# Kernel optimization log

Hardware: AMD Instinct MI355X
Metric: run time of the kernel (lower is better)

The kernel has to match this reference:

```python
import jax, jax.numpy as jnp
import numpy as np

B, C, N = 8, 128, 4096  # (batch, channels=dim, time); F = N//2+1 = 2049 (odd)


def setup_inputs() -> dict:
    key = jax.random.key(0)
    ks = jax.random.split(key, 7)
    s = 1.0 / np.sqrt(C)
    return {
        "x_in": jax.random.normal(ks[0], (B, C, N), dtype=jnp.float32),
        "W_K": jax.random.normal(ks[1], (C, C), dtype=jnp.float32) * s,
        "b_K": jax.random.normal(ks[2], (C,), dtype=jnp.float32) * s,
        "W_V": jax.random.normal(ks[3], (C, C), dtype=jnp.float32) * s,
        "b_V": jax.random.normal(ks[4], (C,), dtype=jnp.float32) * s,
        "w_high": jax.random.normal(ks[5], (C, 2), dtype=jnp.float32) * 0.02,
        "threshold_param": jax.random.uniform(ks[6], (1,), dtype=jnp.float32) * 0.5,
    }


def reference(x_in, W_K, b_K, W_V, b_V, w_high, threshold_param):
    x = jnp.transpose(x_in, (0, 2, 1)).astype(jnp.float32)  # (B, N, C)
    _, n, c = x.shape
    x_fft = jnp.fft.rfft(x, axis=1, norm="ortho")            # (B, F, C) complex64
    K = jnp.fft.rfft(x @ W_K.T + b_K, axis=1, norm="ortho")  # (B, F, C)
    V = jnp.fft.rfft(x @ W_V.T + b_V, axis=1, norm="ortho")  # (B, F, C)
    scale = c ** (-0.5)
    # complex attention scores (no conjugation, matching torch.matmul(Q, K^T))
    attn = jnp.einsum("bfc,bgc->bfg", x_fft, K) * scale      # (B, F, F) complex
    attn = jax.nn.softmax(jnp.abs(attn), axis=-1)            # real softmax of |scores|
    context = jnp.einsum("bfg,bgc->bfc", attn.astype(x_fft.dtype), V)
    # adaptive high-frequency mask
    energy = jnp.sum(jnp.abs(x_fft) ** 2, axis=-1)           # (B, F)
    median_energy = jnp.median(energy, axis=1, keepdims=True)
    normalized = energy / (median_energy + 1e-6)
    threshold = jnp.quantile(normalized, threshold_param[0])  # global quantile
    mask = (normalized > threshold)[:, :, None]               # (B, F, 1)
    w_hi = w_high[:, 0] + 1j * w_high[:, 1]                   # (C,) complex
    context = context + jnp.where(mask, x_fft, 0.0) * w_hi
    out = jnp.fft.irfft(context, n=n, axis=1, norm="ortho")  # (B, N, C) float32
    return jnp.transpose(out, (0, 2, 1))                      # (B, C, N)
```

## Files before the change

### kernel.cpp

```cpp
#include <hip/hip_runtime.h>
#include <math.h>

#define NB 8
#define NC 128
#define NT 4096
#define NF 2049
#define FP 2176

typedef __bf16 bf16;
typedef __bf16 bf16x2 __attribute__((ext_vector_type(2)));
typedef __bf16 bf16x8 __attribute__((ext_vector_type(8)));
typedef float f32x4 __attribute__((ext_vector_type(4)));
typedef unsigned int uint32x4 __attribute__((ext_vector_type(4)));

__device__ __forceinline__ void async16(const bf16* g, bf16* l) {
    __builtin_amdgcn_global_load_lds(
        (const __attribute__((address_space(1))) void*)g,
        (__attribute__((address_space(3))) void*)l, 16, 0, 0);
}

__device__ __forceinline__ bf16x8 derive_b2(bf16x8 v) {
    uint32x4 u = __builtin_bit_cast(uint32x4, v);
#pragma unroll
    for (int i = 0; i < 4; ++i)
        u[i] = (((u[i] >> 16) | (u[i] << 16)) ^ 0x00008000u);
    return __builtin_bit_cast(bf16x8, u);
}

__device__ __forceinline__ float2 cmulf(float2 a, float2 b) {
    return make_float2(a.x * b.x - a.y * b.y, a.x * b.y + a.y * b.x);
}

__global__ __launch_bounds__(256) void twiddle_kernel(float2* __restrict__ tw) {
    int k = blockIdx.x * 256 + threadIdx.x;
    if (k < 2048) {
        float ang = (float)M_PI * (float)k * (1.0f / 2048.0f);
        float sw, cw;
        __sincosf(ang, &sw, &cw);
        tw[k] = make_float2(cw, -sw);
    }
}

__device__ __forceinline__ void fft4096(float2* buf, const float2* __restrict__ tw) {
    int sh = 0;
#pragma unroll
    for (int s6 = 0; s6 < 6; ++s6) {
        int L = 1 << sh;
        __syncthreads();
        for (int t = threadIdx.x; t < 1024; t += 256) {
            int pos = t & (L - 1);
            int base = ((t >> sh) << (sh + 2)) + pos;
            int k1 = pos << (10 - sh);
            float2 w1 = tw[k1];
            float2 w2 = tw[2 * k1];
            float2 w3 = cmulf(w1, w2);
            float2 x0 = buf[base];
            float2 x1 = cmulf(buf[base + L], w1);
            float2 x2 = cmulf(buf[base + 2 * L], w2);
            float2 x3 = cmulf(buf[base + 3 * L], w3);
            float2 b0 = make_float2(x0.x + x2.x, x0.y + x2.y);
            float2 b1 = make_float2(x0.x - x2.x, x0.y - x2.y);
            float2 b2 = make_float2(x1.x + x3.x, x1.y + x3.y);
            float2 b3 = make_float2(x1.x - x3.x, x1.y - x3.y);
            buf[base]         = make_float2(b0.x + b2.x, b0.y + b2.y);
            buf[base + L]     = make_float2(b1.x + b3.y, b1.y - b3.x);
            buf[base + 2 * L] = make_float2(b0.x - b2.x, b0.y - b2.y);
            buf[base + 3 * L] = make_float2(b1.x - b3.y, b1.y + b3.x);
        }
        sh += 2;
    }
    __syncthreads();
}

__device__ __forceinline__ unsigned dr4(unsigned i) {
    unsigned r = __brev(i) >> 20;
    return ((r & 0x555u) << 1) | ((r & 0xAAAu) >> 1);
}

__global__ __launch_bounds__(256) void fft_fwd_kernel(const float* __restrict__ x_in,
                                                      const float2* __restrict__ tw,
                                                      float2* __restrict__ Xc) {
    __shared__ float2 buf[NT];
    int bc = blockIdx.x;
    const float* xrow = x_in + (size_t)bc * NT;
    for (int i = threadIdx.x; i < NT; i += 256)
        buf[dr4((unsigned)i)] = make_float2(xrow[i], 0.0f);
    fft4096(buf, tw);
    const float inv = 1.0f / 64.0f;
    float2* orow = Xc + (size_t)bc * NF;
    for (int f = threadIdx.x; f < NF; f += 256) {
        float2 v = buf[f];
        orow[f] = make_float2(v.x * inv, v.y * inv);
    }
}

__global__ __launch_bounds__(256) void xt_kernel(const float2* __restrict__ Xc,
                                                 float2* __restrict__ Xf2,
                                                 bf16* __restrict__ Xb,
                                                 float* __restrict__ Ep) {
    __shared__ float2 tile[64][65];
    int blk = blockIdx.x;
    int b = blk / 68;
    int t2 = blk % 68;
    int chalf = t2 / 34;
    int c0 = chalf * 64;
    int f0 = (t2 % 34) * 64;
    int t = threadIdx.x;
    int fl = t & 63, cc = t >> 6;
#pragma unroll
    for (int cb = 0; cb < 16; ++cb) {
        int cl = cb * 4 + cc;
        int f = f0 + fl;
        float2 v = make_float2(0.f, 0.f);
        if (f < NF) v = Xc[((size_t)b * NC + c0 + cl) * NF + f];
        tile[fl][cl] = v;
    }
    __syncthreads();
    int chl = t & 63, ww = t >> 6;
    float epart[16];
#pragma unroll
    for (int wb = 0; wb < 16; ++wb) {
        int fl2 = wb * 4 + ww;
        int f = f0 + fl2;
        float2 v = tile[fl2][chl];
        epart[wb] = v.x * v.x + v.y * v.y;
        if (f < NF) Xf2[((size_t)b * NF + f) * 128 + c0 + chl] = v;
        bf16x2 p;
        p[0] = (bf16)v.x; p[1] = (bf16)v.y;
        *(bf16x2*)&Xb[((size_t)b * FP + f) * 256 + 2 * (c0 + chl)] = p;
    }
    __syncthreads();
    float* es = (float*)tile;
#pragma unroll
    for (int wb = 0; wb < 16; ++wb)
        es[(wb * 4 + ww) * 65 + chl] = epart[wb];
    __syncthreads();
    if (t < 64 && f0 + t < NF) {
        float s = 0.f;
#pragma unroll
        for (int c = 0; c < 64; ++c) s += es[t * 65 + c];
        Ep[((size_t)b * 2 + chalf) * FP + f0 + t] = s;
    }
}

__global__ __launch_bounds__(256) void wpack_kernel(const float* __restrict__ W_K,
                                                    const float* __restrict__ W_V,
                                                    bf16* __restrict__ Wk1,
                                                    bf16* __restrict__ Av) {
    int idx = blockIdx.x * 256 + threadIdx.x;
    if (idx < 256 * 256) {
        int n = idx >> 8, k = idx & 255;
        int c = k >> 1;
        int j = n >> 1;
        float v = 0.f;
        if (!(n & 1) && !(k & 1)) v = W_K[j * NC + c];
        else if ((n & 1) && (k & 1)) v = -W_K[j * NC + c];
        Wk1[idx] = (bf16)v;
        float v2 = 0.f;
        if (!(n & 1) && !(k & 1)) v2 = W_V[j * NC + c];
        else if ((n & 1) && (k & 1)) v2 = W_V[j * NC + c];
        Av[idx] = (bf16)v2;
    }
}

__global__ __launch_bounds__(256, 2) void kvgemm_kernel(const bf16* __restrict__ Xb,
                                                        const bf16* __restrict__ Wk1,
                                                        bf16* __restrict__ K1) {
    __shared__ __align__(16) bf16 As[128 * 64];
    __shared__ __align__(16) bf16 Bs[128 * 64];
    int blk = blockIdx.x;
    int b = blk & 7;
    int t2 = blk >> 3;
    int g0 = (t2 >> 1) * 128;
    int n0 = (t2 & 1) * 128;
    int tid = threadIdx.x;
    int wave = tid >> 6, lane = tid & 63;
    int m = lane & 15, quad = lane >> 4;
    int row_off = (wave & 1) * 64, col_off = (wave >> 1) * 64;
    int lrow = lane >> 3;
    int cswz = (lane & 7) ^ lrow;
    int mk = m & 7;

    f32x4 acc[4][4] = {};
    const bf16* Abase = Xb + ((size_t)b * FP + g0) * 256;
    const bf16* Bbase = Wk1 + (size_t)n0 * 256;

    for (int kk = 0; kk < 256; kk += 64) {
        __syncthreads();
#pragma unroll
        for (int t = 0; t < 4; ++t) {
            int r0 = wave * 32 + t * 8;
            async16(Abase + (size_t)(r0 + lrow) * 256 + kk + cswz * 8, As + r0 * 64);
            async16(Bbase + (size_t)(r0 + lrow) * 256 + kk + cswz * 8, Bs + r0 * 64);
        }
        __syncthreads();
#pragma unroll
        for (int k2 = 0; k2 < 64; k2 += 32) {
            bf16x8 a[4], bb[4];
            int pos = (((k2 >> 3) + quad) ^ mk) << 3;
#pragma unroll
            for (int i = 0; i < 4; ++i) a[i] = *(const bf16x8*)&As[(row_off + i * 16 + m) * 64 + pos];
#pragma unroll
            for (int j = 0; j < 4; ++j) bb[j] = *(const bf16x8*)&Bs[(col_off + j * 16 + m) * 64 + pos];
#pragma unroll
            for (int i = 0; i < 4; ++i)
#pragma unroll
                for (int j = 0; j < 4; ++j)
                    acc[i][j] = __builtin_amdgcn_mfma_f32_16x16x32_bf16(a[i], bb[j], acc[i][j], 0, 0, 0);
        }
    }
#pragma unroll
    for (int i = 0; i < 4; ++i)
#pragma unroll
        for (int j = 0; j < 4; ++j)
#pragma unroll
            for (int r = 0; r < 4; ++r) {
                int row = g0 + row_off + i * 16 + quad * 4 + r;
                int col = n0 + col_off + j * 16 + m;
                K1[((size_t)b * FP + row) * 256 + col] = (bf16)acc[i][j][r];
            }
}

__global__ __launch_bounds__(256, 2) void vtgemm_kernel(const bf16* __restrict__ Av,
                                                        const bf16* __restrict__ Xb,
                                                        bf16* __restrict__ Vt) {
    __shared__ __align__(16) bf16 As[128 * 64];
    __shared__ __align__(16) bf16 Bs[128 * 64];
    int blk = blockIdx.x;
    int b = blk & 7;
    int t2 = blk >> 3;
    int g0 = (t2 >> 1) * 128;
    int n0 = (t2 & 1) * 128;
    int tid = threadIdx.x;
    int wave = tid >> 6, lane = tid & 63;
    int m = lane & 15, quad = lane >> 4;
    int row_off = (wave & 1) * 64, col_off = (wave >> 1) * 64;
    int lrow = lane >> 3;
    int cswz = (lane & 7) ^ lrow;
    int mk = m & 7;

    f32x4 acc[4][4] = {};
    const bf16* Abase = Av + (size_t)n0 * 256;
    const bf16* Bbase = Xb + ((size_t)b * FP + g0) * 256;

    for (int kk = 0; kk < 256; kk += 64) {
        __syncthreads();
#pragma unroll
        for (int t = 0; t < 4; ++t) {
            int r0 = wave * 32 + t * 8;
            async16(Abase + (size_t)(r0 + lrow) * 256 + kk + cswz * 8, As + r0 * 64);
            async16(Bbase + (size_t)(r0 + lrow) * 256 + kk + cswz * 8, Bs + r0 * 64);
        }
        __syncthreads();
#pragma unroll
        for (int k2 = 0; k2 < 64; k2 += 32) {
            bf16x8 a[4], bb[4];
            int pos = (((k2 >> 3) + quad) ^ mk) << 3;
#pragma unroll
            for (int i = 0; i < 4; ++i) a[i] = *(const bf16x8*)&As[(row_off + i * 16 + m) * 64 + pos];
#pragma unroll
            for (int j = 0; j < 4; ++j) bb[j] = *(const bf16x8*)&Bs[(col_off + j * 16 + m) * 64 + pos];
#pragma unroll
            for (int i = 0; i < 4; ++i)
#pragma unroll
                for (int j = 0; j < 4; ++j)
                    acc[i][j] = __builtin_amdgcn_mfma_f32_16x16x32_bf16(a[i], bb[j], acc[i][j], 0, 0, 0);
        }
    }
#pragma unroll
    for (int i = 0; i < 4; ++i)
#pragma unroll
        for (int j = 0; j < 4; ++j)
#pragma unroll
            for (int r = 0; r < 4; ++r) {
                int row = n0 + row_off + i * 16 + quad * 4 + r;
                int col = g0 + col_off + j * 16 + m;
                Vt[((size_t)b * 256 + row) * FP + col] = (bf16)acc[i][j][r];
            }
}

__global__ __launch_bounds__(128) void biasfix_kernel(const float* __restrict__ b_K,
                                                      const float* __restrict__ b_V,
                                                      bf16* __restrict__ K1,
                                                      bf16* __restrict__ Vt) {
    int b = blockIdx.x;
    int j = threadIdx.x;
    float bk = 64.0f * b_K[j], bv = 64.0f * b_V[j];
    size_t o = (size_t)b * FP * 256;
    K1[o + 2 * j] = (bf16)((float)K1[o + 2 * j] + bk);
    size_t ov = ((size_t)b * 256 + 2 * j) * FP;
    Vt[ov] = (bf16)((float)Vt[ov] + bv);
}

__global__ __launch_bounds__(256) void median_kernel(const float* __restrict__ Ep,
                                                     float* __restrict__ med) {
    int blk = blockIdx.x;
    int b = blk / 9, chunk = blk % 9;
    __shared__ __align__(16) float e[2052];
    const float* e0 = Ep + (size_t)b * 2 * FP;
    const float* e1 = e0 + FP;
    for (int i = threadIdx.x; i < 2052; i += 256)
        e[i] = (i < NF) ? (e0[i] + e1[i]) : INFINITY;
    __syncthreads();
    int i = chunk * 256 + threadIdx.x;
    float ei = (i < NF) ? e[i] : 0.f;
    int rank = 0;
#pragma unroll 4
    for (int j4 = 0; j4 < 513; ++j4) {
        float4 v = ((const float4*)e)[j4];
        int j = j4 * 4;
        rank += (v.x < ei) || (v.x == ei && j + 0 < i);
        rank += (v.y < ei) || (v.y == ei && j + 1 < i);
        rank += (v.z < ei) || (v.z == ei && j + 2 < i);
        rank += (v.w < ei) || (v.w == ei && j + 3 < i);
    }
    if (i < NF && rank == 1024) med[b] = ei;
}

__global__ __launch_bounds__(256) void norm_kernel(const float* __restrict__ Ep,
                                                   const float* __restrict__ med,
                                                   float* __restrict__ nrm) {
    int idx = blockIdx.x * 256 + threadIdx.x;
    if (idx >= NB * NF) return;
    int b = idx / NF, f = idx % NF;
    float e = Ep[((size_t)b * 2) * FP + f] + Ep[((size_t)b * 2 + 1) * FP + f];
    nrm[idx] = e / (med[b] + 1e-6f);
}

__global__ __launch_bounds__(256) void rankpart_kernel(const float* __restrict__ nrm,
                                                       int* __restrict__ rankpart) {
    const int n = NB * NF;
    int cb = blockIdx.x / 17;
    int chunk = blockIdx.x % 17;
    __shared__ __align__(16) float cdata[1024];
    int base = chunk * 1024;
    for (int t = threadIdx.x; t < 1024; t += 256)
        cdata[t] = (base + t < n) ? nrm[base + t] : INFINITY;
    __syncthreads();
    int i = cb * 256 + threadIdx.x;
    if (i >= n) return;
    float ei = nrm[i];
    int rank = 0;
#pragma unroll 8
    for (int t4 = 0; t4 < 256; ++t4) {
        float4 v = ((const float4*)cdata)[t4];
        int j = base + t4 * 4;
        rank += (v.x < ei) || (v.x == ei && j + 0 < i);
        rank += (v.y < ei) || (v.y == ei && j + 1 < i);
        rank += (v.z < ei) || (v.z == ei && j + 2 < i);
        rank += (v.w < ei) || (v.w == ei && j + 3 < i);
    }
    rankpart[(size_t)i * 17 + chunk] = rank;
}

__global__ __launch_bounds__(256) void rankreduce_kernel(const int* __restrict__ rankpart,
                                                         const float* __restrict__ nrm,
                                                         const float* __restrict__ q,
                                                         float* __restrict__ vk) {
    const int n = NB * NF;
    int i = blockIdx.x * 256 + threadIdx.x;
    if (i >= n) return;
    int rank = 0;
    const int* rp = rankpart + (size_t)i * 17;
#pragma unroll
    for (int c = 0; c < 17; ++c) rank += rp[c];
    double pos = (double)q[0] * (double)(n - 1);
    int k0 = (int)floor(pos);
    int k1 = min(k0 + 1, n - 1);
    if (rank == k0) vk[0] = nrm[i];
    if (rank == k1) vk[1] = nrm[i];
}

__global__ void thresh_kernel(const float* __restrict__ vk,
                              const float* __restrict__ q,
                              float* __restrict__ thr) {
    if (threadIdx.x == 0 && blockIdx.x == 0) {
        const int n = NB * NF;
        double pos = (double)q[0] * (double)(n - 1);
        double k0 = floor(pos);
        double frac = pos - k0;
        thr[0] = (float)((double)vk[0] + ((double)vk[1] - (double)vk[0]) * frac);
    }
}

__global__ __launch_bounds__(256, 3) void score_kernel(const bf16* __restrict__ Xb,
                                                       const bf16* __restrict__ K1,
                                                       bf16* __restrict__ S,
                                                       float* __restrict__ Mpart,
                                                       float* __restrict__ Lpart) {
    __shared__ __align__(16) char smem[24576];
    bf16* As  = (bf16*)smem;
    bf16* B1s = (bf16*)(smem + 16384);
    int blk = blockIdx.x;
    int b = blk & 7;
    int t2 = blk >> 3;
    int f0 = (t2 / 34) * 128;
    int gblk = t2 % 34;
    int g0 = gblk * 64;
    int tid = threadIdx.x;
    int wave = tid >> 6, lane = tid & 63;
    int m = lane & 15, quad = lane >> 4;
    int row_off = (wave & 1) * 64, col_off = (wave >> 1) * 32;

    f32x4 accRe[4][2] = {};
    f32x4 accIm[4][2] = {};
    const bf16* Abase = Xb + ((size_t)b * FP + f0) * 256;
    const bf16* Kbase = K1 + ((size_t)b * FP + g0) * 256;
    int lrow = lane >> 3;
    int cswz = (lane & 7) ^ lrow;
    int mk = m & 7;

    for (int kk = 0; kk < 256; kk += 64) {
        __syncthreads();
#pragma unroll
        for (int t = 0; t < 4; ++t) {
            int r0 = wave * 32 + t * 8;
            async16(Abase + (size_t)(r0 + lrow) * 256 + kk + cswz * 8, As + r0 * 64);
        }
#pragma unroll
        for (int t = 0; t < 2; ++t) {
            int r0 = wave * 16 + t * 8;
            async16(Kbase + (size_t)(r0 + lrow) * 256 + kk + cswz * 8, B1s + r0 * 64);
        }
        __syncthreads();
#pragma unroll
        for (int k2 = 0; k2 < 64; k2 += 32) {
            bf16x8 a[4], b1[2], b2[2];
            int pos = (((k2 >> 3) + quad) ^ mk) << 3;
#pragma unroll
            for (int i = 0; i < 4; ++i)
                a[i] = *(const bf16x8*)&As[(row_off + i * 16 + m) * 64 + pos];
#pragma unroll
            for (int j = 0; j < 2; ++j) {
                b1[j] = *(const bf16x8*)&B1s[(col_off + j * 16 + m) * 64 + pos];
                b2[j] = derive_b2(b1[j]);
            }
#pragma unroll
            for (int i = 0; i < 4; ++i)
#pragma unroll
                for (int j = 0; j < 2; ++j) {
                    accRe[i][j] = __builtin_amdgcn_mfma_f32_16x16x32_bf16(a[i], b1[j], accRe[i][j], 0, 0, 0);
                    accIm[i][j] = __builtin_amdgcn_mfma_f32_16x16x32_bf16(a[i], b2[j], accIm[i][j], 0, 0, 0);
                }
        }
    }
    const float SCALE = 0.08838834764831845f;
    __syncthreads();
    bf16 (*Cs)[76] = (bf16(*)[76])smem;
#pragma unroll
    for (int i = 0; i < 4; ++i)
#pragma unroll
        for (int j = 0; j < 2; ++j)
#pragma unroll
            for (int r = 0; r < 4; ++r) {
                float re = accRe[i][j][r], im = accIm[i][j][r];
                Cs[row_off + i * 16 + quad * 4 + r][col_off + j * 16 + m] =
                    (bf16)(sqrtf(re * re + im * im) * SCALE);
            }
    __syncthreads();
    float* mred = (float*)(smem + 19456);
    float* lred = (float*)(smem + 20480);
    bf16* Sb = S + (size_t)b * FP * FP;
    int row = tid >> 1, half = tid & 1;
    const bf16* src = &Cs[row][half * 32];
    bf16* dst = Sb + (size_t)(f0 + row) * FP + g0 + half * 32;
    int gbase = g0 + half * 32;
    float vf[32];
#pragma unroll
    for (int u = 0; u < 4; ++u) {
        bf16x8 v8 = *(const bf16x8*)&src[u * 8];
        *(bf16x8*)&dst[u * 8] = v8;
#pragma unroll
        for (int e = 0; e < 8; ++e) vf[u * 8 + e] = (float)v8[e];
    }
    if (gblk >= 32) {
#pragma unroll
        for (int k = 0; k < 32; ++k)
            if (gbase + k > 2048) vf[k] = -1e30f;
    }
    float lmax = -1e30f;
#pragma unroll
    for (int k = 0; k < 32; ++k) lmax = fmaxf(lmax, vf[k]);
    mred[tid] = lmax;
    __syncthreads();
    float rmax = fmaxf(mred[row * 2], mred[row * 2 + 1]);
    float lsum = 0.f;
#pragma unroll
    for (int k = 0; k < 32; ++k) lsum += __expf(vf[k] - rmax);
    lred[tid] = lsum;
    __syncthreads();
    if (half == 0) {
        size_t ro = ((size_t)b * FP + f0 + row) * 34 + gblk;
        Mpart[ro] = rmax;
        Lpart[ro] = lred[row * 2] + lred[row * 2 + 1];
    }
}

__global__ __launch_bounds__(256) void rowstat_kernel(const float* __restrict__ Mpart,
                                                      const float* __restrict__ Lpart,
                                                      float* __restrict__ Crow) {
    int row = blockIdx.x * 256 + threadIdx.x;
    if (row >= NB * FP) return;
    const float* mp = Mpart + (size_t)row * 34;
    const float* lp = Lpart + (size_t)row * 34;
    float M = -1e30f;
#pragma unroll
    for (int i = 0; i < 34; ++i) M = fmaxf(M, mp[i]);
    float L = 0.f;
#pragma unroll
    for (int i = 0; i < 34; ++i) L += lp[i] * __expf(mp[i] - M);
    Crow[row] = M + __logf(L);
}

__global__ __launch_bounds__(256) void context_kernel(const bf16* __restrict__ Sg,
                                                      const float* __restrict__ Crow,
                                                      const bf16* __restrict__ Vt,
                                                      float* __restrict__ Ctx) {
    __shared__ __align__(16) bf16 Ps[32 * 64];
    __shared__ __align__(16) bf16 Vs[256 * 64];
    int blk = blockIdx.x;
    int b = blk & 7;
    int f0 = (blk >> 3) * 32;
    int tid = threadIdx.x;
    int wave = tid >> 6, lane = tid & 63;
    int m = lane & 15, quad = lane >> 4;
    int col_off = wave * 64;
    int lrow = lane >> 3;
    int cswz = (lane & 7) ^ lrow;
    int mk = m & 7;

    f32x4 acc[2][4] = {};
    int prow = wave * 8 + lrow;
    const bf16* Prow = Sg + ((size_t)b * FP + f0 + prow) * FP;
    float cst = Crow[(size_t)b * FP + f0 + prow];
    const bf16* Vbase = Vt + (size_t)b * 256 * FP;

    for (int kk = 0; kk < FP; kk += 64) {
        __syncthreads();
#pragma unroll
        for (int t = 0; t < 8; ++t) {
            int r0 = wave * 64 + t * 8;
            async16(Vbase + (size_t)(r0 + lrow) * FP + kk + cswz * 8, Vs + r0 * 64);
        }
        {
            bf16x8 s8 = *(const bf16x8*)&Prow[kk + cswz * 8];
            bf16x8 p8;
#pragma unroll
            for (int e = 0; e < 8; ++e) p8[e] = (bf16)__expf((float)s8[e] - cst);
            *(bf16x8*)&Ps[prow * 64 + (lane & 7) * 8] = p8;
        }
        __syncthreads();
#pragma unroll
        for (int k2 = 0; k2 < 64; k2 += 32) {
            bf16x8 a[2], bb[4];
            int pos = (((k2 >> 3) + quad) ^ mk) << 3;
#pragma unroll
            for (int i = 0; i < 2; ++i) a[i] = *(const bf16x8*)&Ps[(i * 16 + m) * 64 + pos];
#pragma unroll
            for (int j = 0; j < 4; ++j) bb[j] = *(const bf16x8*)&Vs[(col_off + j * 16 + m) * 64 + pos];
#pragma unroll
            for (int i = 0; i < 2; ++i)
#pragma unroll
                for (int j = 0; j < 4; ++j)
                    acc[i][j] = __builtin_amdgcn_mfma_f32_16x16x32_bf16(a[i], bb[j], acc[i][j], 0, 0, 0);
        }
    }
#pragma unroll
    for (int i = 0; i < 2; ++i)
#pragma unroll
        for (int j = 0; j < 4; ++j)
#pragma unroll
            for (int r = 0; r < 4; ++r) {
                int row = f0 + i * 16 + quad * 4 + r;
                int col = col_off + j * 16 + m;
                if (row < NF) Ctx[((size_t)b * NF + row) * 256 + col] = acc[i][j][r];
            }
}

__global__ __launch_bounds__(256) void ctxt_kernel(const float2* __restrict__ Ctx2,
                                                   const float2* __restrict__ Xf2,
                                                   const float* __restrict__ nrm,
                                                   const float* __restrict__ thr,
                                                   const float* __restrict__ w_high,
                                                   float* __restrict__ Ctxt) {
    __shared__ float2 tile[64][33];
    int blk = blockIdx.x;
    int b = blk / 132;
    int t2 = blk % 132;
    int cp0 = (t2 / 33) * 32;
    int f0 = (t2 % 33) * 64;
    int t = threadIdx.x;
    float thrv = thr[0];
    int cpl = t & 31, rr = t >> 5;
#pragma unroll
    for (int rb = 0; rb < 8; ++rb) {
        int fl = rb * 8 + rr;
        int f = f0 + fl;
        float2 v = make_float2(0.f, 0.f);
        if (f < NF) {
            size_t idx = ((size_t)b * NF + f) * 128 + cp0 + cpl;
            v = Ctx2[idx];
            if (nrm[b * NF + f] > thrv) {
                float2 x = Xf2[idx];
                int c = cp0 + cpl;
                float wr = w_high[2 * c], wi = w_high[2 * c + 1];
                v.x += x.x * wr - x.y * wi;
                v.y += x.x * wi + x.y * wr;
            }
        }
        tile[fl][cpl] = v;
    }
    __syncthreads();
    int fl = t & 63, ww = t >> 6;
#pragma unroll
    for (int wb = 0; wb < 16; ++wb) {
        int chl = wb * 4 + ww;
        int f = f0 + fl;
        if (f < NF) {
            float2 v = tile[fl][chl >> 1];
            Ctxt[((size_t)b * 256 + 2 * cp0 + chl) * NF + f] = (chl & 1) ? v.y : v.x;
        }
    }
}

__global__ __launch_bounds__(256) void fft_inv_kernel(const float* __restrict__ Ctxt,
                                                      const float2* __restrict__ tw,
                                                      float* __restrict__ out) {
    __shared__ float2 buf[NT];
    int bc = blockIdx.x, b = bc >> 7, c = bc & 127;
    const float* base = Ctxt + ((size_t)b * 256 + 2 * c) * NF;
    const float* basei = base + NF;
    for (int f = threadIdx.x; f < NT; f += 256) {
        float re, im;
        if (f <= NT / 2) {
            re = base[f];
            im = -basei[f];
        } else {
            int g = NT - f;
            re = base[g];
            im = basei[g];
        }
        buf[dr4((unsigned)f)] = make_float2(re, im);
    }
    fft4096(buf, tw);
    float* orow = out + (size_t)bc * NT;
    const float inv = 1.0f / 64.0f;
    for (int n = threadIdx.x; n < NT; n += 256) orow[n] = buf[n].x * inv;
}

extern "C" void kernel_launch(void* const* d_in, const int* in_sizes, int n_in,
                              void* d_out, int out_size, void* d_ws, size_t ws_size,
                              hipStream_t stream) {
    const float* x_in = (const float*)d_in[0];
    const float* W_K = (const float*)d_in[1];
    const float* b_K = (const float*)d_in[2];
    const float* W_V = (const float*)d_in[3];
    const float* b_V = (const float*)d_in[4];
    const float* w_high = (const float*)d_in[5];
    const float* qpar = (const float*)d_in[6];
    float* out = (float*)d_out;

    char* w = (char*)d_ws;
    const size_t SPECB = (size_t)NB * NF * 256 * 4;
    float* Xf = (float*)w;            w += SPECB;
    float* Ctx = (float*)w;           w += SPECB;
    float* Ep = (float*)w;            w += (size_t)NB * 2 * FP * 4;
    float* med = (float*)w;           w += 64;
    float* nrm = (float*)w;           w += (size_t)NB * NF * 4;
    float* vk = (float*)w;            w += 64;
    float* thr = (float*)w;           w += 64;
    w = (char*)(((uintptr_t)w + 255) & ~(uintptr_t)255);
    float2* tw = (float2*)w;          w += (size_t)2048 * 8;
    int* rankpart = (int*)w;          w += (size_t)16640 * 17 * 4;
    w = (char*)(((uintptr_t)w + 255) & ~(uintptr_t)255);
    float* Mpart = (float*)w;         w += (size_t)NB * FP * 34 * 4;
    float* Lpart = (float*)w;         w += (size_t)NB * FP * 34 * 4;
    float* Crow = (float*)w;          w += (size_t)NB * FP * 4;
    w = (char*)(((uintptr_t)w + 255) & ~(uintptr_t)255);
    bf16* S = (bf16*)w;               w += (size_t)NB * FP * FP * 2;
    bf16* Xb = (bf16*)w;              w += (size_t)NB * FP * 256 * 2;
    bf16* K1 = (bf16*)w;              w += (size_t)NB * FP * 256 * 2;
    bf16* Vt = (bf16*)w;              w += (size_t)NB * 256 * FP * 2;
    bf16* Wk1 = (bf16*)w;             w += (size_t)256 * 256 * 2;
    bf16* Av = (bf16*)w;              w += (size_t)256 * 256 * 2;
    float2* Xc = (float2*)S;
    float* Ctxt = (float*)Xb;

    twiddle_kernel<<<8, 256, 0, stream>>>(tw);
    fft_fwd_kernel<<<NB * NC, 256, 0, stream>>>(x_in, tw, Xc);
    xt_kernel<<<NB * 2 * 34, 256, 0, stream>>>(Xc, (float2*)Xf, Xb, Ep);
    wpack_kernel<<<256, 256, 0, stream>>>(W_K, W_V, Wk1, Av);
    kvgemm_kernel<<<NB * 17 * 2, 256, 0, stream>>>(Xb, Wk1, K1);
    vtgemm_kernel<<<NB * 17 * 2, 256, 0, stream>>>(Av, Xb, Vt);
    biasfix_kernel<<<NB, 128, 0, stream>>>(b_K, b_V, K1, Vt);
    median_kernel<<<NB * 9, 256, 0, stream>>>(Ep, med);
    norm_kernel<<<(NB * NF + 255) / 256, 256, 0, stream>>>(Ep, med, nrm);
    rankpart_kernel<<<65 * 17, 256, 0, stream>>>(nrm, rankpart);
    rankreduce_kernel<<<65, 256, 0, stream>>>(rankpart, nrm, qpar, vk);
    thresh_kernel<<<1, 64, 0, stream>>>(vk, qpar, thr);
    score_kernel<<<NB * 17 * 34, 256, 0, stream>>>(Xb, K1, S, Mpart, Lpart);
    rowstat_kernel<<<(NB * FP + 255) / 256, 256, 0, stream>>>(Mpart, Lpart, Crow);
    context_kernel<<<NB * 65, 256, 0, stream>>>(S, Crow, Vt, Ctx);
    ctxt_kernel<<<NB * 4 * 33, 256, 0, stream>>>((const float2*)Ctx, (const float2*)Xf,
                                                 nrm, thr, w_high, Ctxt);
    fft_inv_kernel<<<NB * NC, 256, 0, stream>>>(Ctxt, tw, out);
}
```

Baseline: 394.2 us.

## Fuse high-freq mask and transpose into context epilogue, fold bias and prep kernels

The context GEMM epilogue now applies the masked high-frequency term and transposes through shared memory. It writes the channel-major Ctxt buffer directly, so the separate ctxt pass and the full-size float Ctx intermediate are gone, along with that buffer's global write and read-back. Bias addition moves into the K/V GEMM epilogues, and the twiddle and weight-pack kernels merge into one prep kernel, removing three launches. The trade-off is extra per-element branching in the GEMM epilogues and a shared-memory transpose stage in the context kernel.

```diff
diff --git a/kernel.cpp b/kernel.cpp
--- a/kernel.cpp
+++ b/kernel.cpp
@@ -31,14 +31,29 @@
     return make_float2(a.x * b.x - a.y * b.y, a.x * b.y + a.y * b.x);
 }
 
-__global__ __launch_bounds__(256) void twiddle_kernel(float2* __restrict__ tw) {
-    int k = blockIdx.x * 256 + threadIdx.x;
-    if (k < 2048) {
-        float ang = (float)M_PI * (float)k * (1.0f / 2048.0f);
+__global__ __launch_bounds__(256) void prep_kernel(const float* __restrict__ W_K,
+                                                   const float* __restrict__ W_V,
+                                                   float2* __restrict__ tw,
+                                                   bf16* __restrict__ Wk1,
+                                                   bf16* __restrict__ Av) {
+    int idx = blockIdx.x * 256 + threadIdx.x;
+    if (idx < 2048) {
+        float ang = (float)M_PI * (float)idx * (1.0f / 2048.0f);
         float sw, cw;
         __sincosf(ang, &sw, &cw);
-        tw[k] = make_float2(cw, -sw);
-    }
+        tw[idx] = make_float2(cw, -sw);
+    }
+    int n = idx >> 8, k = idx & 255;
+    int c = k >> 1;
+    int j = n >> 1;
+    float v = 0.f;
+    if (!(n & 1) && !(k & 1)) v = W_K[j * NC + c];
+    else if ((n & 1) && (k & 1)) v = -W_K[j * NC + c];
+    Wk1[idx] = (bf16)v;
+    float v2 = 0.f;
+    if (!(n & 1) && !(k & 1)) v2 = W_V[j * NC + c];
+    else if ((n & 1) && (k & 1)) v2 = W_V[j * NC + c];
+    Av[idx] = (bf16)v2;
 }
 
 __device__ __forceinline__ void fft4096(float2* buf, const float2* __restrict__ tw) {
@@ -143,28 +158,9 @@
     }
 }
 
-__global__ __launch_bounds__(256) void wpack_kernel(const float* __restrict__ W_K,
-                                                    const float* __restrict__ W_V,
-                                                    bf16* __restrict__ Wk1,
-                                                    bf16* __restrict__ Av) {
-    int idx = blockIdx.x * 256 + threadIdx.x;
-    if (idx < 256 * 256) {
-        int n = idx >> 8, k = idx & 255;
-        int c = k >> 1;
-        int j = n >> 1;
-        float v = 0.f;
-        if (!(n & 1) && !(k & 1)) v = W_K[j * NC + c];
-        else if ((n & 1) && (k & 1)) v = -W_K[j * NC + c];
-        Wk1[idx] = (bf16)v;
-        float v2 = 0.f;
-        if (!(n & 1) && !(k & 1)) v2 = W_V[j * NC + c];
-        else if ((n & 1) && (k & 1)) v2 = W_V[j * NC + c];
-        Av[idx] = (bf16)v2;
-    }
-}
-
 __global__ __launch_bounds__(256, 2) void kvgemm_kernel(const bf16* __restrict__ Xb,
                                                         const bf16* __restrict__ Wk1,
+                                                        const float* __restrict__ b_K,
                                                         bf16* __restrict__ K1) {
     __shared__ __align__(16) bf16 As[128 * 64];
     __shared__ __align__(16) bf16 Bs[128 * 64];
@@ -217,12 +213,15 @@
             for (int r = 0; r < 4; ++r) {
                 int row = g0 + row_off + i * 16 + quad * 4 + r;
                 int col = n0 + col_off + j * 16 + m;
-                K1[((size_t)b * FP + row) * 256 + col] = (bf16)acc[i][j][r];
+                float val = acc[i][j][r];
+                if (row == 0 && !(col & 1)) val += 64.0f * b_K[col >> 1];
+                K1[((size_t)b * FP + row) * 256 + col] = (bf16)val;
             }
 }
 
 __global__ __launch_bounds__(256, 2) void vtgemm_kernel(const bf16* __restrict__ Av,
                                                         const bf16* __restrict__ Xb,
+                                                        const float* __restrict__ b_V,
                                                         bf16* __restrict__ Vt) {
     __shared__ __align__(16) bf16 As[128 * 64];
     __shared__ __align__(16) bf16 Bs[128 * 64];
@@ -275,21 +274,10 @@
             for (int r = 0; r < 4; ++r) {
                 int row = n0 + row_off + i * 16 + quad * 4 + r;
                 int col = g0 + col_off + j * 16 + m;
-                Vt[((size_t)b * 256 + row) * FP + col] = (bf16)acc[i][j][r];
+                float val = acc[i][j][r];
+                if (col == 0 && !(row & 1)) val += 64.0f * b_V[row >> 1];
+                Vt[((size_t)b * 256 + row) * FP + col] = (bf16)val;
             }
-}
-
-__global__ __launch_bounds__(128) void biasfix_kernel(const float* __restrict__ b_K,
-                                                      const float* __restrict__ b_V,
-                                                      bf16* __restrict__ K1,
-                                                      bf16* __restrict__ Vt) {
-    int b = blockIdx.x;
-    int j = threadIdx.x;
-    float bk = 64.0f * b_K[j], bv = 64.0f * b_V[j];
-    size_t o = (size_t)b * FP * 256;
-    K1[o + 2 * j] = (bf16)((float)K1[o + 2 * j] + bk);
-    size_t ov = ((size_t)b * 256 + 2 * j) * FP;
-    Vt[ov] = (bf16)((float)Vt[ov] + bv);
 }
 
 __global__ __launch_bounds__(256) void median_kernel(const float* __restrict__ Ep,
@@ -515,9 +503,14 @@
 __global__ __launch_bounds__(256) void context_kernel(const bf16* __restrict__ Sg,
                                                       const float* __restrict__ Crow,
                                                       const bf16* __restrict__ Vt,
-                                                      float* __restrict__ Ctx) {
-    __shared__ __align__(16) bf16 Ps[32 * 64];
-    __shared__ __align__(16) bf16 Vs[256 * 64];
+                                                      const float2* __restrict__ Xf2,
+                                                      const float* __restrict__ nrm,
+                                                      const float* __restrict__ thr,
+                                                      const float* __restrict__ w_high,
+                                                      float* __restrict__ Ctxt) {
+    __shared__ __align__(16) char smem[36864];
+    bf16* Ps = (bf16*)smem;
+    bf16* Vs = (bf16*)(smem + 4096);
     int blk = blockIdx.x;
     int b = blk & 7;
     int f0 = (blk >> 3) * 32;
@@ -565,60 +558,44 @@
                     acc[i][j] = __builtin_amdgcn_mfma_f32_16x16x32_bf16(a[i], bb[j], acc[i][j], 0, 0, 0);
         }
     }
+    float thrv = thr[0];
 #pragma unroll
     for (int i = 0; i < 2; ++i)
 #pragma unroll
+        for (int r = 0; r < 4; ++r) {
+            int row = f0 + i * 16 + quad * 4 + r;
+            if (row < NF && nrm[b * NF + row] > thrv) {
+#pragma unroll
+                for (int j = 0; j < 4; ++j) {
+                    int col = col_off + j * 16 + m;
+                    int c = col >> 1;
+                    float2 x = Xf2[((size_t)b * NF + row) * 128 + c];
+                    float wr = w_high[2 * c], wi = w_high[2 * c + 1];
+                    acc[i][j][r] += (col & 1) ? (x.x * wi + x.y * wr)
+                                              : (x.x * wr - x.y * wi);
+                }
+            }
+        }
+    __syncthreads();
+    float (*Ts)[33] = (float(*)[33])smem;
+#pragma unroll
+    for (int i = 0; i < 2; ++i)
+#pragma unroll
         for (int j = 0; j < 4; ++j)
 #pragma unroll
             for (int r = 0; r < 4; ++r) {
-                int row = f0 + i * 16 + quad * 4 + r;
+                int fl = i * 16 + quad * 4 + r;
                 int col = col_off + j * 16 + m;
-                if (row < NF) Ctx[((size_t)b * NF + row) * 256 + col] = acc[i][j][r];
+                Ts[col][fl] = acc[i][j][r];
             }
-}
-
-__global__ __launch_bounds__(256) void ctxt_kernel(const float2* __restrict__ Ctx2,
-                                                   const float2* __restrict__ Xf2,
-                                                   const float* __restrict__ nrm,
-                                                   const float* __restrict__ thr,
-                                                   const float* __restrict__ w_high,
-                                                   float* __restrict__ Ctxt) {
-    __shared__ float2 tile[64][33];
-    int blk = blockIdx.x;
-    int b = blk / 132;
-    int t2 = blk % 132;
-    int cp0 = (t2 / 33) * 32;
-    int f0 = (t2 % 33) * 64;
-    int t = threadIdx.x;
-    float thrv = thr[0];
-    int cpl = t & 31, rr = t >> 5;
-#pragma unroll
-    for (int rb = 0; rb < 8; ++rb) {
-        int fl = rb * 8 + rr;
-        int f = f0 + fl;
-        float2 v = make_float2(0.f, 0.f);
-        if (f < NF) {
-            size_t idx = ((size_t)b * NF + f) * 128 + cp0 + cpl;
-            v = Ctx2[idx];
-            if (nrm[b * NF + f] > thrv) {
-                float2 x = Xf2[idx];
-                int c = cp0 + cpl;
-                float wr = w_high[2 * c], wi = w_high[2 * c + 1];
-                v.x += x.x * wr - x.y * wi;
-                v.y += x.x * wi + x.y * wr;
-            }
-        }
-        tile[fl][cpl] = v;
-    }
-    __syncthreads();
-    int fl = t & 63, ww = t >> 6;
-#pragma unroll
-    for (int wb = 0; wb < 16; ++wb) {
-        int chl = wb * 4 + ww;
-        int f = f0 + fl;
-        if (f < NF) {
-            float2 v = tile[fl][chl >> 1];
-            Ctxt[((size_t)b * 256 + 2 * cp0 + chl) * NF + f] = (chl & 1) ? v.y : v.x;
+    __syncthreads();
+    int f = tid & 31;
+    int ch0 = tid >> 5;
+    if (f0 + f < NF) {
+#pragma unroll
+        for (int p = 0; p < 32; ++p) {
+            int ch = ch0 + p * 8;
+            Ctxt[((size_t)b * 256 + ch) * NF + f0 + f] = Ts[ch][f];
         }
     }
 }
@@ -663,7 +640,6 @@
     char* w = (char*)d_ws;
     const size_t SPECB = (size_t)NB * NF * 256 * 4;
     float* Xf = (float*)w;            w += SPECB;
-    float* Ctx = (float*)w;           w += SPECB;
     float* Ep = (float*)w;            w += (size_t)NB * 2 * FP * 4;
     float* med = (float*)w;           w += 64;
     float* nrm = (float*)w;           w += (size_t)NB * NF * 4;
@@ -686,13 +662,11 @@
     float2* Xc = (float2*)S;
     float* Ctxt = (float*)Xb;
 
-    twiddle_kernel<<<8, 256, 0, stream>>>(tw);
+    prep_kernel<<<256, 256, 0, stream>>>(W_K, W_V, tw, Wk1, Av);
     fft_fwd_kernel<<<NB * NC, 256, 0, stream>>>(x_in, tw, Xc);
     xt_kernel<<<NB * 2 * 34, 256, 0, stream>>>(Xc, (float2*)Xf, Xb, Ep);
-    wpack_kernel<<<256, 256, 0, stream>>>(W_K, W_V, Wk1, Av);
-    kvgemm_kernel<<<NB * 17 * 2, 256, 0, stream>>>(Xb, Wk1, K1);
-    vtgemm_kernel<<<NB * 17 * 2, 256, 0, stream>>>(Av, Xb, Vt);
-    biasfix_kernel<<<NB, 128, 0, stream>>>(b_K, b_V, K1, Vt);
+    kvgemm_kernel<<<NB * 17 * 2, 256, 0, stream>>>(Xb, Wk1, b_K, K1);
+    vtgemm_kernel<<<NB * 17 * 2, 256, 0, stream>>>(Av, Xb, b_V, Vt);
     median_kernel<<<NB * 9, 256, 0, stream>>>(Ep, med);
     norm_kernel<<<(NB * NF + 255) / 256, 256, 0, stream>>>(Ep, med, nrm);
     rankpart_kernel<<<65 * 17, 256, 0, stream>>>(nrm, rankpart);
@@ -700,8 +674,7 @@
     thresh_kernel<<<1, 64, 0, stream>>>(vk, qpar, thr);
     score_kernel<<<NB * 17 * 34, 256, 0, stream>>>(Xb, K1, S, Mpart, Lpart);
     rowstat_kernel<<<(NB * FP + 255) / 256, 256, 0, stream>>>(Mpart, Lpart, Crow);
-    context_kernel<<<NB * 65, 256, 0, stream>>>(S, Crow, Vt, Ctx);
-    ctxt_kernel<<<NB * 4 * 33, 256, 0, stream>>>((const float2*)Ctx, (const float2*)Xf,
-                                                 nrm, thr, w_high, Ctxt);
+    context_kernel<<<NB * 65, 256, 0, stream>>>(S, Crow, Vt, (const float2*)Xf,
+                                                nrm, thr, w_high, Ctxt);
     fft_inv_kernel<<<NB * NC, 256, 0, stream>>>(Ctxt, tw, out);
 }
```

Measured after the change: 389.1 us. About the same (-1.3%).
